# Optimization experiments

Measured on AMD Instinct MI355X. Metric: run time of the kernel, lower is better.

## Reference

```python
import jax, jax.numpy as jnp
from jax import lax
import numpy as np

# 6D tensors: (N, C, h1, w1, h2, w2); weights: (Cout, Cin, k,k,k,k)
DN = lax.ConvDimensionNumbers(lhs_spec=(0, 1, 2, 3, 4, 5),
                              rhs_spec=(0, 1, 2, 3, 4, 5),
                              out_spec=(0, 1, 2, 3, 4, 5))


def conv4d_relu(x, w, b):
    # true 4D convolution, stride 1, SAME padding, then bias + ReLU
    y = lax.conv_general_dilated(x, w, window_strides=(1, 1, 1, 1),
                                 padding='SAME', dimension_numbers=DN)
    return jax.nn.relu(y + b.reshape(1, -1, 1, 1, 1, 1))


def _perm(x):
    # swap the two (h, w) spatial pairs of the correlation tensor
    return jnp.transpose(x, (0, 1, 4, 5, 2, 3))


def _sym(x, w, b):
    # symmetric_mode branch: f(x) + perm(f(perm(x)))
    return conv4d_relu(x, w, b) + _perm(conv4d_relu(_perm(x), w, b))


def setup_inputs() -> dict:
    key = jax.random.key(0)
    ks = jax.random.split(key, 9)
    B, S = 4, 20
    sc = 0.05
    return {
        'x':    jax.random.normal(ks[0], (B, 1, S, S, S, S), dtype=jnp.float32),
        'w0':   jax.random.normal(ks[1], (16, 1, 5, 5, 5, 5), dtype=jnp.float32) * sc,
        'b0':   jax.random.normal(ks[2], (16,), dtype=jnp.float32) * sc,
        'w10':  jax.random.normal(ks[3], (8, 16, 3, 3, 5, 5), dtype=jnp.float32) * sc,
        'b10':  jax.random.normal(ks[4], (8,), dtype=jnp.float32) * sc,
        'w11':  jax.random.normal(ks[5], (8, 16, 5, 5, 5, 5), dtype=jnp.float32) * sc,
        'b11':  jax.random.normal(ks[6], (8,), dtype=jnp.float32) * sc,
        'w2':   jax.random.normal(ks[7], (1, 16, 5, 5, 5, 5), dtype=jnp.float32) * sc,
        'b2':   jax.random.normal(ks[8], (1,), dtype=jnp.float32) * sc,
    }


def reference(x, w0, b0, w10, b10, w11, b11, w2, b2):
    x = _sym(x, w0, b0)                       # [B,16,S,S,S,S]
    x0 = _sym(x, w10, b10)                    # [B, 8,S,S,S,S]
    x1 = _sym(x, w11, b11)                    # [B, 8,S,S,S,S]
    x = jnp.concatenate((x0, x1), axis=1)     # [B,16,S,S,S,S]
    return _sym(x, w2, b2)                    # [B, 1,S,S,S,S]
```

## Files before the change

### kernel.cpp

```cpp
#include <hip/hip_runtime.h>

#define TS 20
#define TS2 400

typedef __attribute__((ext_vector_type(8))) __bf16 bf16x8;
typedef __attribute__((ext_vector_type(4))) __bf16 bf16x4;
typedef __attribute__((ext_vector_type(4))) float  f32x4;
typedef __attribute__((ext_vector_type(4))) int    int4v;

__device__ __forceinline__ float relu_f(float v) { return v > 0.0f ? v : 0.0f; }

#define MFMA16(a, b, c) __builtin_amdgcn_mfma_f32_16x16x32_bf16((a), (b), (c), 0, 0, 0)

#define LPAD 580

__global__ __launch_bounds__(256)
void pack_w0(const float* __restrict__ w0, __bf16* __restrict__ wpk0)
{
    int idx = blockIdx.x * 256 + (int)threadIdx.x;
    if (idx >= 25 * 32 * 32) return;
    const int c = idx & 31;
    const int m = (idx >> 5) & 31;
    const int e = idx >> 10;
    float v = 0.0f;
    if (c < 25) {
        const int co = m & 15;
        const int k1o = c / 5, k2o = c % 5, k3i = e / 5, k4i = e % 5;
        if (m < 16) v = w0[co * 625 + k1o * 125 + k2o * 25 + k3i * 5 + k4i];
        else        v = w0[co * 625 + k3i * 125 + k4i * 25 + k1o * 5 + k2o];
    }
    wpk0[idx] = (__bf16)v;
}

__global__ __launch_bounds__(256)
void pack_wmid(const float* __restrict__ w10, const float* __restrict__ w11,
               __bf16* __restrict__ wpk)
{
    int idx = blockIdx.x * 256 + (int)threadIdx.x;
    if (idx >= 650 * 512) return;
    const int ci  = idx & 15;
    const int m   = (idx >> 4) & 31;
    const int off = idx >> 9;
    const int inner = off % 26, outer = off / 26;
    const int d1 = outer / 5 - 2, d2 = outer % 5 - 2;
    float v = 0.0f;
    if (inner < 25) {
        const int d3 = inner / 5 - 2, d4 = inner % 5 - 2;
        const int co = m & 7;
        const bool isB  = (m & 8)  != 0;
        const bool is11 = (m & 16) != 0;
        if (is11) {
            int k1, k2, k3, k4;
            if (!isB) { k1 = d1 + 2; k2 = d2 + 2; k3 = d3 + 2; k4 = d4 + 2; }
            else      { k1 = d3 + 2; k2 = d4 + 2; k3 = d1 + 2; k4 = d2 + 2; }
            v = w11[((((co * 16 + ci) * 5 + k1) * 5 + k2) * 5 + k3) * 5 + k4];
        } else {
            if (!isB) {
                if (d1 >= -1 && d1 <= 1 && d2 >= -1 && d2 <= 1)
                    v = w10[((((co * 16 + ci) * 3 + (d1 + 1)) * 3 + (d2 + 1)) * 5 + (d3 + 2)) * 5 + (d4 + 2)];
            } else {
                if (d3 >= -1 && d3 <= 1 && d4 >= -1 && d4 <= 1)
                    v = w10[((((co * 16 + ci) * 3 + (d3 + 1)) * 3 + (d4 + 1)) * 5 + (d1 + 2)) * 5 + (d2 + 2)];
            }
        }
    }
    wpk[idx] = (__bf16)v;
}

__global__ __launch_bounds__(256)
void pack_w2f(const float* __restrict__ w2, __bf16* __restrict__ wpk2f)
{
    int idx = blockIdx.x * 256 + (int)threadIdx.x;
    if (idx >= 26 * 64 * 16) return;
    const int ci = idx & 15;
    const int m  = (idx >> 4) & 63;
    const int e  = idx >> 10;
    float v = 0.0f;
    if (e < 25) {
        if (m < 25)
            v = w2[ci * 625 + (m / 5) * 125 + (m % 5) * 25 + (e / 5) * 5 + (e % 5)];
        else if (m >= 32 && m < 57) {
            const int dd = m - 32;
            v = w2[ci * 625 + (e / 5) * 125 + (e % 5) * 25 + (dd / 5) * 5 + (dd % 5)];
        }
    }
    wpk2f[idx] = (__bf16)v;
}

__global__ __launch_bounds__(320)
void conv0_mfma(const float* __restrict__ x, const __bf16* __restrict__ wpk0,
                const float* __restrict__ b0, __bf16* __restrict__ y1)
{
    __shared__ __bf16 lds0[4 * LPAD * 8];

    const int tid  = (int)threadIdx.x;
    const int lane = tid & 63;
    const int wave = tid >> 6;
    const int bid  = blockIdx.x;
    const int o2 = bid % TS, o1 = (bid / TS) % TS, n = bid / TS2;

    for (int i = tid; i < 4 * LPAD * 8 / 2; i += 320) ((int*)lds0)[i] = 0;
    __syncthreads();

    for (int c = tid; c < 25 * TS2; c += 320) {
        const int pl = c / TS2, pt = c % TS2;
        const int i1 = o1 + pl / 5 - 2, i2 = o2 + pl % 5 - 2;
        if (i1 >= 0 && i1 < TS && i2 >= 0 && i2 < TS) {
            const float v = x[(size_t)((n * TS + i1) * TS + i2) * TS2 + pt];
            const int L = (pt / TS + 2) * 24 + (pt % TS + 2);
            lds0[((pl >> 3) * LPAD + L) * 8 + (pl & 7)] = (__bf16)v;
        }
    }
    __syncthreads();

    const int mrow = lane & 15;
    const int sub  = lane >> 4;

    int sb[5];
#pragma unroll
    for (int i = 0; i < 5; ++i) {
        const int p = (wave * 5 + i) * 16 + mrow;
        sb[i] = (sub * LPAD + (p / TS + 2) * 24 + (p % TS + 2)) * 8;
    }

    f32x4 acc0[5], acc1[5];
#pragma unroll
    for (int i = 0; i < 5; ++i) {
        acc0[i] = (f32x4){0.f, 0.f, 0.f, 0.f};
        acc1[i] = (f32x4){0.f, 0.f, 0.f, 0.f};
    }

    bf16x8 a0 = *(const bf16x8*)(wpk0 + (size_t)mrow * 32 + sub * 8);
    bf16x8 a1 = *(const bf16x8*)(wpk0 + (size_t)(16 + mrow) * 32 + sub * 8);
    for (int e = 0; e < 25; ++e) {
        bf16x8 na0 = a0, na1 = a1;
        if (e < 24) {
            na0 = *(const bf16x8*)(wpk0 + ((size_t)((e + 1) * 32 + mrow)) * 32 + sub * 8);
            na1 = *(const bf16x8*)(wpk0 + ((size_t)((e + 1) * 32 + 16 + mrow)) * 32 + sub * 8);
        }
        const int delta = ((e / 5 - 2) * 24 + (e % 5 - 2)) * 8;
#pragma unroll
        for (int i = 0; i < 5; ++i) {
            bf16x8 bfr = *(const bf16x8*)(&lds0[sb[i] + delta]);
            acc0[i] = MFMA16(a0, bfr, acc0[i]);
            acc1[i] = MFMA16(a1, bfr, acc1[i]);
        }
        a0 = na0; a1 = na1;
    }

    const f32x4 bv = *(const f32x4*)(b0 + sub * 4);
#pragma unroll
    for (int i = 0; i < 5; ++i) {
        const int p = (wave * 5 + i) * 16 + mrow;
        bf16x4 pk;
#pragma unroll
        for (int r = 0; r < 4; ++r)
            pk[r] = (__bf16)(relu_f(acc0[i][r] + bv[r]) + relu_f(acc1[i][r] + bv[r]));
        *(bf16x4*)(y1 + ((size_t)bid * TS2 + p) * 16 + sub * 4) = pk;
    }
}

__global__ __launch_bounds__(320)
void conv4d_mid_mfma(const __bf16* __restrict__ y1, const __bf16* __restrict__ wpk,
                     const float* __restrict__ b10, const float* __restrict__ b11,
                     __bf16* __restrict__ y2)
{
    __shared__ __bf16 lds[2][9216];

    const int tid  = (int)threadIdx.x;
    const int lane = tid & 63;
    const int wave = tid >> 6;
    const int bid0 = blockIdx.x;
    const int bid  = (bid0 & 7) * 200 + (bid0 >> 3);
    const int o2 = bid % TS, o1 = (bid / TS) % TS, n = bid / TS2;

    for (int i = tid; i < 9216; i += 320) ((int*)lds)[i] = 0;

    const int mrow = lane & 15;
    const int sub  = lane >> 4;
    const int ci0  = (sub & 1) * 8;
    const int aoff = (sub >> 1) * 512 + mrow * 16 + ci0;

    const int wo0 = ((tid / 40 + 2) * 24 + 2) * 16 + (tid % 40) * 8;
    const int wo1 = (((tid + 320) / 40 + 2) * 24 + 2) * 16 + ((tid + 320) % 40) * 8;
    const int wo2 = (((tid + 640) / 40 + 2) * 24 + 2) * 16 + ((tid + 640) % 40) * 8;
    const bool c2ok = tid < 160;
    const __bf16* ybase = y1 + (size_t)n * TS2 * TS2 * 16;

    int sbase[5];
#pragma unroll
    for (int i = 0; i < 5; ++i) {
        const int p  = (wave * 5 + i) * 16 + mrow;
        sbase[i] = ((p / TS + 2) * 24 + (p % TS + 2)) * 16 + ci0;
    }

    f32x4 acc[5][2];
#pragma unroll
    for (int i = 0; i < 5; ++i) {
        acc[i][0] = (f32x4){0.f, 0.f, 0.f, 0.f};
        acc[i][1] = (f32x4){0.f, 0.f, 0.f, 0.f};
    }

    int kk = 0;
    {
        while (kk < 25) {
            const int i1 = o1 + kk / 5 - 2, i2 = o2 + kk % 5 - 2;
            if (i1 >= 0 && i1 < TS && i2 >= 0 && i2 < TS) break;
            ++kk;
        }
    }
    int4v s0, s1, s2;
    {
        const int i1 = o1 + kk / 5 - 2, i2 = o2 + kk % 5 - 2;
        const __bf16* src = ybase + (size_t)(i1 * TS + i2) * TS2 * 16;
        s0 = *(const int4v*)(src + tid * 8);
        s1 = *(const int4v*)(src + (tid + 320) * 8);
        if (c2ok) s2 = *(const int4v*)(src + (tid + 640) * 8);
    }
    __syncthreads();

    int buf = 0;
    while (kk < 25) {
        *(int4v*)(&lds[buf][wo0]) = s0;
        *(int4v*)(&lds[buf][wo1]) = s1;
        if (c2ok) *(int4v*)(&lds[buf][wo2]) = s2;
        __syncthreads();

        int nk = kk + 1;
        while (nk < 25) {
            const int i1 = o1 + nk / 5 - 2, i2 = o2 + nk % 5 - 2;
            if (i1 >= 0 && i1 < TS && i2 >= 0 && i2 < TS) break;
            ++nk;
        }
        if (nk < 25) {
            const int i1 = o1 + nk / 5 - 2, i2 = o2 + nk % 5 - 2;
            const __bf16* src = ybase + (size_t)(i1 * TS + i2) * TS2 * 16;
            s0 = *(const int4v*)(src + tid * 8);
            s1 = *(const int4v*)(src + (tid + 320) * 8);
            if (c2ok) s2 = *(const int4v*)(src + (tid + 640) * 8);
        }

        const __bf16* wbase = wpk + (size_t)kk * 26 * 512;
        bf16x8 a0 = *(const bf16x8*)(wbase + aoff);
        bf16x8 a1 = *(const bf16x8*)(wbase + aoff + 256);
        __builtin_amdgcn_s_setprio(1);
        for (int ic = 0; ic < 13; ++ic) {
            bf16x8 na0 = a0, na1 = a1;
            if (ic < 12) {
                na0 = *(const bf16x8*)(wbase + (ic + 1) * 1024 + aoff);
                na1 = *(const bf16x8*)(wbase + (ic + 1) * 1024 + aoff + 256);
            }
            const int e = 2 * ic + (sub >> 1);
            int d3 = 0, d4 = 0;
            if (e < 25) { d3 = e / 5 - 2; d4 = e % 5 - 2; }
            const int delta = (d3 * 24 + d4) * 16;
#pragma unroll
            for (int i = 0; i < 5; ++i) {
                bf16x8 bfr = *(const bf16x8*)(&lds[buf][sbase[i] + delta]);
                acc[i][0] = MFMA16(a0, bfr, acc[i][0]);
                acc[i][1] = MFMA16(a1, bfr, acc[i][1]);
            }
            a0 = na0; a1 = na1;
        }
        __builtin_amdgcn_s_setprio(0);

        buf ^= 1;
        kk = nk;
    }

    const size_t base = (size_t)bid * TS2 * 16;
#pragma unroll
    for (int i = 0; i < 5; ++i) {
        const int p = (wave * 5 + i) * 16 + mrow;
#pragma unroll
        for (int mt = 0; mt < 2; ++mt) {
            const float* bs = mt ? b11 : b10;
            const f32x4 bv = *(const f32x4*)(bs + (sub & 1) * 4);
            bf16x4 pk;
#pragma unroll
            for (int r = 0; r < 4; ++r) {
                float v = relu_f(acc[i][mt][r] + bv[r]);
                float o = v + __shfl_xor(v, 32);
                pk[r] = (__bf16)o;
            }
            if (lane < 32)
                *(bf16x4*)(y2 + base + (size_t)p * 16 + mt * 8 + (sub & 1) * 4) = pk;
        }
    }
}

__global__ __launch_bounds__(320)
void conv2t_mfma(const __bf16* __restrict__ y2, const __bf16* __restrict__ wpk2f,
                 int n0, __bf16* __restrict__ t)
{
    __shared__ __bf16 lds[2 * LPAD * 8];

    const int tid  = (int)threadIdx.x;
    const int lane = tid & 63;
    const int wave = tid >> 6;
    const int bid = blockIdx.x;
    const int q2 = bid % TS, q1 = (bid / TS) % TS, nl = bid / TS2;

    for (int i = tid; i < 2 * LPAD * 8 / 2; i += 320) ((int*)lds)[i] = 0;
    __syncthreads();

    const __bf16* src = y2 + (size_t)(((n0 + nl) * TS + q1) * TS + q2) * TS2 * 16;
    for (int c = tid; c < 800; c += 320) {
        const int h = c / 40, rem = c % 40;
        const int w = rem >> 1, cb = rem & 1;
        int4v v = *(const int4v*)(src + c * 8);
        *(int4v*)(&lds[(cb * LPAD + (h + 2) * 24 + 2 + w) * 8]) = v;
    }
    __syncthreads();

    const int mrow = lane & 15;
    const int sub  = lane >> 4;

    int sbase[5];
#pragma unroll
    for (int i = 0; i < 5; ++i) {
        const int p  = (wave * 5 + i) * 16 + mrow;
        sbase[i] = ((sub & 1) * LPAD + (p / TS + 2) * 24 + (p % TS + 2)) * 8;
    }

    f32x4 acc[5][4];
#pragma unroll
    for (int i = 0; i < 5; ++i)
#pragma unroll
        for (int mt = 0; mt < 4; ++mt)
            acc[i][mt] = (f32x4){0.f, 0.f, 0.f, 0.f};

    for (int ic = 0; ic < 13; ++ic) {
        const int e = 2 * ic + (sub >> 1);
        int d3 = 0, d4 = 0;
        if (e < 25) { d3 = e / 5 - 2; d4 = e % 5 - 2; }
        const int delta = (d3 * 24 + d4) * 8;
        const __bf16* abase = wpk2f + ((size_t)e * 64 + mrow) * 16 + (sub & 1) * 8;
        bf16x8 a0 = *(const bf16x8*)(abase);
        bf16x8 a1 = *(const bf16x8*)(abase + 256);
        bf16x8 a2 = *(const bf16x8*)(abase + 512);
        bf16x8 a3 = *(const bf16x8*)(abase + 768);
#pragma unroll
        for (int i = 0; i < 5; ++i) {
            bf16x8 bfr = *(const bf16x8*)(&lds[sbase[i] + delta]);
            acc[i][0] = MFMA16(a0, bfr, acc[i][0]);
            acc[i][1] = MFMA16(a1, bfr, acc[i][1]);
            acc[i][2] = MFMA16(a2, bfr, acc[i][2]);
            acc[i][3] = MFMA16(a3, bfr, acc[i][3]);
        }
    }

    __bf16* tb = t + (size_t)((nl * TS + q1) * TS + q2) * (50 * TS2);
#pragma unroll
    for (int i = 0; i < 5; ++i) {
        const int p = (wave * 5 + i) * 16 + mrow;
#pragma unroll
        for (int mt = 0; mt < 4; ++mt) {
#pragma unroll
            for (int r = 0; r < 4; ++r) {
                const int gm = mt * 16 + sub * 4 + r;
                int m50 = -1;
                if (gm < 25) m50 = gm;
                else if (gm >= 32 && gm < 57) m50 = gm - 7;
                if (m50 >= 0) tb[m50 * TS2 + p] = (__bf16)acc[i][mt][r];
            }
        }
    }
}

__global__ __launch_bounds__(448)
void conv2_sum(const __bf16* __restrict__ t, const float* __restrict__ b2,
               int n0, float* __restrict__ out)
{
    const int tid = (int)threadIdx.x;
    if (tid >= TS2) return;
    const int bid = blockIdx.x;
    const int o2 = bid % TS, o1 = (bid / TS) % TS, nl = bid / TS2;

    float accA = 0.0f, accB = 0.0f;
    for (int dd = 0; dd < 25; ++dd) {
        const int q1 = o1 + dd / 5 - 2, q2 = o2 + dd % 5 - 2;
        if (q1 < 0 || q1 >= TS || q2 < 0 || q2 >= TS) continue;
        const __bf16* tb = t + (size_t)((nl * TS + q1) * TS + q2) * (50 * TS2) + tid;
        accA += (float)tb[dd * TS2];
        accB += (float)tb[(25 + dd) * TS2];
    }
    const float bias = b2[0];
    out[(size_t)(n0 + nl) * (TS2 * (size_t)TS2) + (size_t)(o1 * TS + o2) * TS2 + tid] =
        relu_f(accA + bias) + relu_f(accB + bias);
}

extern "C" void kernel_launch(void* const* d_in, const int* in_sizes, int n_in,
                              void* d_out, int out_size, void* d_ws, size_t ws_size,
                              hipStream_t stream)
{
    const float* x   = (const float*)d_in[0];
    const float* w0  = (const float*)d_in[1];
    const float* b0  = (const float*)d_in[2];
    const float* w10 = (const float*)d_in[3];
    const float* b10 = (const float*)d_in[4];
    const float* w11 = (const float*)d_in[5];
    const float* b11 = (const float*)d_in[6];
    const float* w2  = (const float*)d_in[7];
    const float* b2  = (const float*)d_in[8];
    float* out = (float*)d_out;

    __bf16* y1    = (__bf16*)d_ws;
    __bf16* y2    = y1 + (size_t)10240000;
    __bf16* tbuf  = y2 + (size_t)10240000;
    __bf16* wpkm  = tbuf + (size_t)16000000;
    __bf16* wpk0  = wpkm + 650 * 512;
    __bf16* wpk2f = wpk0 + 25 * 32 * 32;

    dim3 blk320(320), blk256(256), blk448(448);

    pack_w0  <<<dim3((25600 + 255) / 256),  blk256, 0, stream>>>(w0, wpk0);
    pack_wmid<<<dim3((332800 + 255) / 256), blk256, 0, stream>>>(w10, w11, wpkm);
    pack_w2f <<<dim3((26624 + 255) / 256),  blk256, 0, stream>>>(w2, wpk2f);

    conv0_mfma     <<<dim3(4 * TS * TS), blk320, 0, stream>>>(x, wpk0, b0, y1);
    conv4d_mid_mfma<<<dim3(1600),        blk320, 0, stream>>>(y1, wpkm, b10, b11, y2);

    for (int n0 = 0; n0 < 4; n0 += 2) {
        conv2t_mfma<<<dim3(800), blk320, 0, stream>>>(y2, wpk2f, n0, tbuf);
        conv2_sum  <<<dim3(800), blk448, 0, stream>>>(tbuf, b2, n0, out);
    }
}
```

Baseline: 495.7 us.

## Store y1 pre-padded and stream planes into LDS with direct global-to-LDS loads

conv0 now writes y1 into a zero-padded 24x24x16 plane layout, and a separate kernel zeroes that buffer first. conv4d_mid can then copy whole padded planes straight into LDS with global_load_lds, with no register staging, per-block LDS zeroing or index remapping. The loads for the next plane are issued before compute and a barrier closes each iteration. The setprio hints are dropped, and the conv2 stage now runs once per batch item with a smaller tbuf. The cost is extra memory traffic for the padded buffer and its zero-fill pass.

```diff
diff --git a/kernel.cpp b/kernel.cpp
--- a/kernel.cpp
+++ b/kernel.cpp
@@ -2,6 +2,7 @@
 
 #define TS 20
 #define TS2 400
+#define PLANE 9216
 
 typedef __attribute__((ext_vector_type(8))) __bf16 bf16x8;
 typedef __attribute__((ext_vector_type(4))) __bf16 bf16x4;
@@ -11,6 +12,13 @@
 __device__ __forceinline__ float relu_f(float v) { return v > 0.0f ? v : 0.0f; }
 
 #define MFMA16(a, b, c) __builtin_amdgcn_mfma_f32_16x16x32_bf16((a), (b), (c), 0, 0, 0)
+
+__device__ __forceinline__ void gload_lds16(const __bf16* g, __bf16* l)
+{
+    __builtin_amdgcn_global_load_lds(
+        (const __attribute__((address_space(1))) void*)g,
+        (__attribute__((address_space(3))) void*)l, 16, 0, 0);
+}
 
 #define LPAD 580
 
@@ -87,6 +95,14 @@
     wpk2f[idx] = (__bf16)v;
 }
 
+__global__ __launch_bounds__(256)
+void zero_y1p(int4v* __restrict__ dst, int n16)
+{
+    const int stride = gridDim.x * 256;
+    for (int i = blockIdx.x * 256 + (int)threadIdx.x; i < n16; i += stride)
+        dst[i] = (int4v){0, 0, 0, 0};
+}
+
 __global__ __launch_bounds__(320)
 void conv0_mfma(const float* __restrict__ x, const __bf16* __restrict__ wpk0,
                 const float* __restrict__ b0, __bf16* __restrict__ y1)
@@ -152,11 +168,12 @@
 #pragma unroll
     for (int i = 0; i < 5; ++i) {
         const int p = (wave * 5 + i) * 16 + mrow;
+        const int Lp = (p / TS + 2) * 24 + (p % TS + 2);
         bf16x4 pk;
 #pragma unroll
         for (int r = 0; r < 4; ++r)
             pk[r] = (__bf16)(relu_f(acc0[i][r] + bv[r]) + relu_f(acc1[i][r] + bv[r]));
-        *(bf16x4*)(y1 + ((size_t)bid * TS2 + p) * 16 + sub * 4) = pk;
+        *(bf16x4*)(y1 + (size_t)bid * PLANE + Lp * 16 + sub * 4) = pk;
     }
 }
 
@@ -165,7 +182,7 @@
                      const float* __restrict__ b10, const float* __restrict__ b11,
                      __bf16* __restrict__ y2)
 {
-    __shared__ __bf16 lds[2][9216];
+    __shared__ __bf16 lds[2][PLANE];
 
     const int tid  = (int)threadIdx.x;
     const int lane = tid & 63;
@@ -174,19 +191,11 @@
     const int bid  = (bid0 & 7) * 200 + (bid0 >> 3);
     const int o2 = bid % TS, o1 = (bid / TS) % TS, n = bid / TS2;
 
-    for (int i = tid; i < 9216; i += 320) ((int*)lds)[i] = 0;
-
     const int mrow = lane & 15;
     const int sub  = lane >> 4;
     const int ci0  = (sub & 1) * 8;
     const int aoff = (sub >> 1) * 512 + mrow * 16 + ci0;
 
-    const int wo0 = ((tid / 40 + 2) * 24 + 2) * 16 + (tid % 40) * 8;
-    const int wo1 = (((tid + 320) / 40 + 2) * 24 + 2) * 16 + ((tid + 320) % 40) * 8;
-    const int wo2 = (((tid + 640) / 40 + 2) * 24 + 2) * 16 + ((tid + 640) % 40) * 8;
-    const bool c2ok = tid < 160;
-    const __bf16* ybase = y1 + (size_t)n * TS2 * TS2 * 16;
-
     int sbase[5];
 #pragma unroll
     for (int i = 0; i < 5; ++i) {
@@ -201,31 +210,23 @@
         acc[i][1] = (f32x4){0.f, 0.f, 0.f, 0.f};
     }
 
+    const __bf16* ybase = y1 + (size_t)n * TS2 * PLANE;
+
     int kk = 0;
+    while (kk < 25) {
+        const int i1 = o1 + kk / 5 - 2, i2 = o2 + kk % 5 - 2;
+        if (i1 >= 0 && i1 < TS && i2 >= 0 && i2 < TS) break;
+        ++kk;
+    }
     {
-        while (kk < 25) {
-            const int i1 = o1 + kk / 5 - 2, i2 = o2 + kk % 5 - 2;
-            if (i1 >= 0 && i1 < TS && i2 >= 0 && i2 < TS) break;
-            ++kk;
-        }
-    }
-    int4v s0, s1, s2;
-    {
-        const int i1 = o1 + kk / 5 - 2, i2 = o2 + kk % 5 - 2;
-        const __bf16* src = ybase + (size_t)(i1 * TS + i2) * TS2 * 16;
-        s0 = *(const int4v*)(src + tid * 8);
-        s1 = *(const int4v*)(src + (tid + 320) * 8);
-        if (c2ok) s2 = *(const int4v*)(src + (tid + 640) * 8);
+        const __bf16* pl = ybase + (size_t)((o1 + kk / 5 - 2) * TS + (o2 + kk % 5 - 2)) * PLANE;
+        for (int i = wave; i < 18; i += 5)
+            gload_lds16(pl + i * 512 + lane * 8, &lds[0][i * 512]);
     }
     __syncthreads();
 
     int buf = 0;
     while (kk < 25) {
-        *(int4v*)(&lds[buf][wo0]) = s0;
-        *(int4v*)(&lds[buf][wo1]) = s1;
-        if (c2ok) *(int4v*)(&lds[buf][wo2]) = s2;
-        __syncthreads();
-
         int nk = kk + 1;
         while (nk < 25) {
             const int i1 = o1 + nk / 5 - 2, i2 = o2 + nk % 5 - 2;
@@ -233,17 +234,14 @@
             ++nk;
         }
         if (nk < 25) {
-            const int i1 = o1 + nk / 5 - 2, i2 = o2 + nk % 5 - 2;
-            const __bf16* src = ybase + (size_t)(i1 * TS + i2) * TS2 * 16;
-            s0 = *(const int4v*)(src + tid * 8);
-            s1 = *(const int4v*)(src + (tid + 320) * 8);
-            if (c2ok) s2 = *(const int4v*)(src + (tid + 640) * 8);
+            const __bf16* pl = ybase + (size_t)((o1 + nk / 5 - 2) * TS + (o2 + nk % 5 - 2)) * PLANE;
+            for (int i = wave; i < 18; i += 5)
+                gload_lds16(pl + i * 512 + lane * 8, &lds[buf ^ 1][i * 512]);
         }
 
         const __bf16* wbase = wpk + (size_t)kk * 26 * 512;
         bf16x8 a0 = *(const bf16x8*)(wbase + aoff);
         bf16x8 a1 = *(const bf16x8*)(wbase + aoff + 256);
-        __builtin_amdgcn_s_setprio(1);
         for (int ic = 0; ic < 13; ++ic) {
             bf16x8 na0 = a0, na1 = a1;
             if (ic < 12) {
@@ -262,8 +260,8 @@
             }
             a0 = na0; a1 = na1;
         }
-        __builtin_amdgcn_s_setprio(0);
-
+
+        __syncthreads();
         buf ^= 1;
         kk = nk;
     }
@@ -405,10 +403,10 @@
     const float* b2  = (const float*)d_in[8];
     float* out = (float*)d_out;
 
-    __bf16* y1    = (__bf16*)d_ws;
-    __bf16* y2    = y1 + (size_t)10240000;
+    __bf16* y1p   = (__bf16*)d_ws;
+    __bf16* y2    = y1p + (size_t)4 * TS2 * PLANE;
     __bf16* tbuf  = y2 + (size_t)10240000;
-    __bf16* wpkm  = tbuf + (size_t)16000000;
+    __bf16* wpkm  = tbuf + (size_t)8000000;
     __bf16* wpk0  = wpkm + 650 * 512;
     __bf16* wpk2f = wpk0 + 25 * 32 * 32;
 
@@ -418,11 +416,13 @@
     pack_wmid<<<dim3((332800 + 255) / 256), blk256, 0, stream>>>(w10, w11, wpkm);
     pack_w2f <<<dim3((26624 + 255) / 256),  blk256, 0, stream>>>(w2, wpk2f);
 
-    conv0_mfma     <<<dim3(4 * TS * TS), blk320, 0, stream>>>(x, wpk0, b0, y1);
-    conv4d_mid_mfma<<<dim3(1600),        blk320, 0, stream>>>(y1, wpkm, b10, b11, y2);
-
-    for (int n0 = 0; n0 < 4; n0 += 2) {
-        conv2t_mfma<<<dim3(800), blk320, 0, stream>>>(y2, wpk2f, n0, tbuf);
-        conv2_sum  <<<dim3(800), blk448, 0, stream>>>(tbuf, b2, n0, out);
-    }
-}
+    zero_y1p<<<dim3(2048), blk256, 0, stream>>>((int4v*)y1p, (int)((size_t)4 * TS2 * PLANE * 2 / 16));
+
+    conv0_mfma     <<<dim3(4 * TS * TS), blk320, 0, stream>>>(x, wpk0, b0, y1p);
+    conv4d_mid_mfma<<<dim3(1600),        blk320, 0, stream>>>(y1p, wpkm, b10, b11, y2);
+
+    for (int n0 = 0; n0 < 4; ++n0) {
+        conv2t_mfma<<<dim3(400), blk320, 0, stream>>>(y2, wpk2f, n0, tbuf);
+        conv2_sum  <<<dim3(400), blk448, 0, stream>>>(tbuf, b2, n0, out);
+    }
+}
```

After: 560.5 us. 1.13x slower.
